# Kernel tuning notes

Hardware: AMD Instinct MI355X
Metric: run time of the kernel (lower is better)

Reference implementation:

```python
import jax, jax.numpy as jnp
import numpy as np

MEM_DIM = 1024
N_CHILD = 16384

def _linear_params(key, out_dim, in_dim):
    kw, kb = jax.random.split(key)
    bound = 1.0 / np.sqrt(in_dim)
    W = jax.random.uniform(kw, (out_dim, in_dim), jnp.float32, -bound, bound)
    b = jax.random.uniform(kb, (out_dim,), jnp.float32, -bound, bound)
    return W, b

def setup_inputs() -> dict:
    key = jax.random.key(0)
    ks = jax.random.split(key, 7)
    child_c = jax.random.normal(ks[0], (N_CHILD, MEM_DIM), jnp.float32)
    child_h = jax.random.normal(ks[1], (N_CHILD, MEM_DIM), jnp.float32)
    child_h_sum = jax.random.normal(ks[2], (MEM_DIM,), jnp.float32)
    W_ih, b_ih = _linear_params(ks[3], MEM_DIM, MEM_DIM)
    W_fh, b_fh = _linear_params(ks[4], MEM_DIM, MEM_DIM)
    W_uh, b_uh = _linear_params(ks[5], MEM_DIM, MEM_DIM)
    W_oh, b_oh = _linear_params(ks[6], MEM_DIM, MEM_DIM)
    return {
        "child_c": child_c, "child_h": child_h, "child_h_sum": child_h_sum,
        "W_ih": W_ih, "b_ih": b_ih, "W_fh": W_fh, "b_fh": b_fh,
        "W_uh": W_uh, "b_uh": b_uh, "W_oh": W_oh, "b_oh": b_oh,
    }

def reference(child_c, child_h, child_h_sum,
              W_ih, b_ih, W_fh, b_fh, W_uh, b_uh, W_oh, b_oh):
    # Gate projections on the summed child hidden state: [mem_dim]
    i = jax.nn.sigmoid(child_h_sum @ W_ih.T + b_ih)
    o = jax.nn.sigmoid(child_h_sum @ W_oh.T + b_oh)
    u = jnp.tanh(child_h_sum @ W_uh.T + b_uh)
    # Per-child forget gates, batched (replaces the Python loop): [N, mem_dim]
    f = jax.nn.sigmoid(child_h @ W_fh.T + b_fh)
    fc = f * child_c                     # [N, mem_dim]
    c = i * u + jnp.sum(fc, axis=0)      # [mem_dim]
    h = o * jnp.tanh(c)                  # [mem_dim]
    return (c, h)
```

## Files before the change

### kernel.cpp

```cpp
#include <hip/hip_runtime.h>
#include <hip/hip_bf16.h>
#include <math.h>

#define MEM_DIM 1024
#define N_CHILD 16384

#define BM 128
#define BN 64
#define BK 64
#define KITERS (MEM_DIM / BK)

typedef __bf16 bf16_t;
typedef __bf16 bf16x4 __attribute__((ext_vector_type(4)));
typedef __bf16 bf16x8 __attribute__((ext_vector_type(8)));
typedef float f32x4 __attribute__((ext_vector_type(4)));

__device__ __forceinline__ void async_load16(const bf16_t* g, bf16_t* l) {
    __builtin_amdgcn_global_load_lds(
        (const __attribute__((address_space(1))) unsigned int*)g,
        (__attribute__((address_space(3))) unsigned int*)l,
        16, 0, 0);
}

__global__ __launch_bounds__(256) void prep_kernel(
        const float* __restrict__ child_h, const float* __restrict__ W_fh,
        bf16_t* __restrict__ dst, int n8,
        const float* __restrict__ hsum,
        const float* __restrict__ W_ih, const float* __restrict__ b_ih,
        const float* __restrict__ W_uh, const float* __restrict__ b_uh,
        const float* __restrict__ W_oh, const float* __restrict__ b_oh,
        float* __restrict__ acc_c, float* __restrict__ o_ws) {
    const int tid = threadIdx.x;
    if (blockIdx.x < MEM_DIM) {
        const int j = blockIdx.x;
        const float* wi = W_ih + (size_t)j * MEM_DIM;
        const float* wu = W_uh + (size_t)j * MEM_DIM;
        const float* wo = W_oh + (size_t)j * MEM_DIM;
        float4 h4  = *(const float4*)(hsum + tid * 4);
        float4 wi4 = *(const float4*)(wi + tid * 4);
        float4 wu4 = *(const float4*)(wu + tid * 4);
        float4 wo4 = *(const float4*)(wo + tid * 4);
        float si = wi4.x * h4.x + wi4.y * h4.y + wi4.z * h4.z + wi4.w * h4.w;
        float su = wu4.x * h4.x + wu4.y * h4.y + wu4.z * h4.z + wu4.w * h4.w;
        float so = wo4.x * h4.x + wo4.y * h4.y + wo4.z * h4.z + wo4.w * h4.w;
        for (int off = 32; off > 0; off >>= 1) {
            si += __shfl_down(si, off, 64);
            su += __shfl_down(su, off, 64);
            so += __shfl_down(so, off, 64);
        }
        __shared__ float red[3][4];
        const int wave = tid >> 6, lane = tid & 63;
        if (lane == 0) { red[0][wave] = si; red[1][wave] = su; red[2][wave] = so; }
        __syncthreads();
        if (tid == 0) {
            float ti = red[0][0] + red[0][1] + red[0][2] + red[0][3] + b_ih[j];
            float tu = red[1][0] + red[1][1] + red[1][2] + red[1][3] + b_uh[j];
            float to = red[2][0] + red[2][1] + red[2][2] + red[2][3] + b_oh[j];
            float iv = 1.f / (1.f + expf(-ti));
            float uv = tanhf(tu);
            float ov = 1.f / (1.f + expf(-to));
            acc_c[j] = iv * uv;
            o_ws[j]  = ov;
        }
    } else {
        const int nA8 = (N_CHILD * MEM_DIM) / 8;
        int t = (blockIdx.x - MEM_DIM) * 256 + tid;
        if (t < n8) {
            const float* s = (t < nA8) ? (child_h + (size_t)t * 8)
                                       : (W_fh + (size_t)(t - nA8) * 8);
            float4 a = *(const float4*)s;
            float4 b = *(const float4*)(s + 4);
            bf16x8 o = { (bf16_t)a.x, (bf16_t)a.y, (bf16_t)a.z, (bf16_t)a.w,
                         (bf16_t)b.x, (bf16_t)b.y, (bf16_t)b.z, (bf16_t)b.w };
            *(bf16x8*)(dst + (size_t)t * 8) = o;
        }
    }
}

__global__ __launch_bounds__(256) void fused_gemm_bf16(
        const bf16_t* __restrict__ hbf, const bf16_t* __restrict__ wbf,
        const float* __restrict__ child_c, const float* __restrict__ b_fh,
        float* __restrict__ acc_c) {
    __shared__ __align__(1024) bf16_t sA[BM * BK];
    __shared__ __align__(1024) bf16_t sB[BN * BK];
    __shared__ float sred[BN];

    const int tid  = threadIdx.x;
    const int lane = tid & 63;
    const int wave = tid >> 6;
    const int wr = wave >> 1;
    const int wc = wave & 1;
    const int q  = lane >> 4;
    const int cl = lane & 15;

    const int b   = blockIdx.x;
    const int xcd = b & 7;
    const int l   = b >> 3;
    const int jt  = l & 15;
    const int ntl = l >> 4;
    const int j0  = jt * BN;
    const int n0  = (xcd * 16 + ntl) * BM;

    const int rl = lane >> 3;
    const int p  = lane & 7;
    const int cf = (p ^ rl) * 8;
    const bf16_t* gA[4];
    bf16_t* lA[4];
#pragma unroll
    for (int i = 0; i < 4; i++) {
        const int r = wave * 32 + i * 8 + rl;
        gA[i] = hbf + (size_t)(n0 + r) * MEM_DIM + cf;
        lA[i] = &sA[(wave * 32 + i * 8) * BK];
    }
    const bf16_t* gB[2];
    bf16_t* lB[2];
#pragma unroll
    for (int i = 0; i < 2; i++) {
        const int r = wave * 16 + i * 8 + rl;
        gB[i] = wbf + (size_t)(j0 + r) * MEM_DIM + cf;
        lB[i] = &sB[(wave * 16 + i * 8) * BK];
    }

    f32x4 acc[4][2];
#pragma unroll
    for (int a = 0; a < 4; a++)
#pragma unroll
        for (int c = 0; c < 2; c++) acc[a][c] = (f32x4)0.0f;

#pragma unroll 1
    for (int k = 0; k < KITERS - 1; ++k) {
#pragma unroll
        for (int i = 0; i < 4; i++) { async_load16(gA[i], lA[i]); gA[i] += BK; }
#pragma unroll
        for (int i = 0; i < 2; i++) { async_load16(gB[i], lB[i]); gB[i] += BK; }
        __syncthreads();

#pragma unroll
        for (int h = 0; h < 2; h++) {
            bf16x8 af[4], bfr[2];
#pragma unroll
            for (int mt = 0; mt < 4; mt++) {
                const int ra = wr * 64 + mt * 16 + cl;
                af[mt] = *(const bf16x8*)(&sA[ra * BK + (((4 * h + q) ^ (cl & 7)) * 8)]);
            }
#pragma unroll
            for (int nt = 0; nt < 2; nt++) {
                const int rb = wc * 32 + nt * 16 + cl;
                bfr[nt] = *(const bf16x8*)(&sB[rb * BK + (((4 * h + q) ^ (cl & 7)) * 8)]);
            }
#pragma unroll
            for (int mt = 0; mt < 4; mt++)
#pragma unroll
                for (int nt = 0; nt < 2; nt++)
                    acc[mt][nt] = __builtin_amdgcn_mfma_f32_16x16x32_bf16(
                        af[mt], bfr[nt], acc[mt][nt], 0, 0, 0);
        }
        __syncthreads();
    }

#pragma unroll
    for (int i = 0; i < 4; i++) async_load16(gA[i], lA[i]);
#pragma unroll
    for (int i = 0; i < 2; i++) async_load16(gB[i], lB[i]);

    float ccr[2][4][4];
    float biasr[2];
    {
        const float* ccp = child_c + (size_t)(n0 + wr * 64 + q * 4) * MEM_DIM
                                   + j0 + wc * 32 + cl;
#pragma unroll
        for (int nt = 0; nt < 2; nt++) {
            biasr[nt] = b_fh[j0 + wc * 32 + nt * 16 + cl];
#pragma unroll
            for (int mt = 0; mt < 4; mt++)
#pragma unroll
                for (int r = 0; r < 4; r++)
                    ccr[nt][mt][r] = ccp[(size_t)(mt * 16 + r) * MEM_DIM + nt * 16];
        }
    }
    __syncthreads();

#pragma unroll
    for (int h = 0; h < 2; h++) {
        bf16x8 af[4], bfr[2];
#pragma unroll
        for (int mt = 0; mt < 4; mt++) {
            const int ra = wr * 64 + mt * 16 + cl;
            af[mt] = *(const bf16x8*)(&sA[ra * BK + (((4 * h + q) ^ (cl & 7)) * 8)]);
        }
#pragma unroll
        for (int nt = 0; nt < 2; nt++) {
            const int rb = wc * 32 + nt * 16 + cl;
            bfr[nt] = *(const bf16x8*)(&sB[rb * BK + (((4 * h + q) ^ (cl & 7)) * 8)]);
        }
#pragma unroll
        for (int mt = 0; mt < 4; mt++)
#pragma unroll
            for (int nt = 0; nt < 2; nt++)
                acc[mt][nt] = __builtin_amdgcn_mfma_f32_16x16x32_bf16(
                    af[mt], bfr[nt], acc[mt][nt], 0, 0, 0);
    }

    if (tid < BN) sred[tid] = 0.0f;
    __syncthreads();

    float colsum[2] = {0.f, 0.f};
#pragma unroll
    for (int nt = 0; nt < 2; nt++) {
#pragma unroll
        for (int mt = 0; mt < 4; mt++) {
#pragma unroll
            for (int r = 0; r < 4; r++) {
                float s = acc[mt][nt][r] + biasr[nt];
                float fg = 1.0f / (1.0f + __expf(-s));
                colsum[nt] += fg * ccr[nt][mt][r];
            }
        }
        colsum[nt] += __shfl_xor(colsum[nt], 16, 64);
        colsum[nt] += __shfl_xor(colsum[nt], 32, 64);
    }
    if (q == 0) {
#pragma unroll
        for (int nt = 0; nt < 2; nt++)
            atomicAdd(&sred[wc * 32 + nt * 16 + cl], colsum[nt]);
    }
    __syncthreads();
    if (tid < BN) atomicAdd(&acc_c[j0 + tid], sred[tid]);
}

__global__ void finalize_kernel(const float* __restrict__ acc_c,
                                const float* __restrict__ o_ws,
                                float* __restrict__ out) {
    int t = blockIdx.x * 256 + threadIdx.x;
    if (t < MEM_DIM) {
        float cv = acc_c[t];
        float hv = o_ws[t] * tanhf(cv);
        out[t] = cv;
        out[MEM_DIM + t] = hv;
    }
}

__global__ void gates_kernel(const float* __restrict__ hsum,
                             const float* __restrict__ W_ih, const float* __restrict__ b_ih,
                             const float* __restrict__ W_uh, const float* __restrict__ b_uh,
                             const float* __restrict__ W_oh, const float* __restrict__ b_oh,
                             float* __restrict__ acc_c, float* __restrict__ o_ws) {
    const int j = blockIdx.x;
    const int tid = threadIdx.x;
    const float* wi = W_ih + (size_t)j * MEM_DIM;
    const float* wu = W_uh + (size_t)j * MEM_DIM;
    const float* wo = W_oh + (size_t)j * MEM_DIM;
    float si = 0.f, su = 0.f, so = 0.f;
    for (int k = tid; k < MEM_DIM; k += 256) {
        float hv = hsum[k];
        si += wi[k] * hv;
        su += wu[k] * hv;
        so += wo[k] * hv;
    }
    for (int off = 32; off > 0; off >>= 1) {
        si += __shfl_down(si, off, 64);
        su += __shfl_down(su, off, 64);
        so += __shfl_down(so, off, 64);
    }
    __shared__ float red[3][4];
    const int wave = tid >> 6, lane = tid & 63;
    if (lane == 0) { red[0][wave] = si; red[1][wave] = su; red[2][wave] = so; }
    __syncthreads();
    if (tid == 0) {
        float ti = red[0][0] + red[0][1] + red[0][2] + red[0][3] + b_ih[j];
        float tu = red[1][0] + red[1][1] + red[1][2] + red[1][3] + b_uh[j];
        float to = red[2][0] + red[2][1] + red[2][2] + red[2][3] + b_oh[j];
        acc_c[j] = (1.f / (1.f + expf(-ti))) * tanhf(tu);
        o_ws[j]  = 1.f / (1.f + expf(-to));
    }
}

#define LDS_STRIDE 40
__global__ __launch_bounds__(256) void fused_gemm_f32(
        const float* __restrict__ child_h, const float* __restrict__ child_c,
        const float* __restrict__ W_fh, const float* __restrict__ b_fh,
        float* __restrict__ acc_c) {
    __shared__ __align__(16) bf16_t sA[128 * LDS_STRIDE];
    __shared__ __align__(16) bf16_t sB[128 * LDS_STRIDE];
    __shared__ float sred[128];
    const int tid = threadIdx.x, lane = tid & 63, wave = tid >> 6;
    const int wr = wave >> 1, wc = wave & 1;
    const int j0 = blockIdx.x * 128, n0 = blockIdx.y * 128;
    const int q = lane >> 4, cl = lane & 15;
    f32x4 acc[4][4];
#pragma unroll
    for (int a = 0; a < 4; a++)
#pragma unroll
        for (int c = 0; c < 4; c++) acc[a][c] = (f32x4)0.0f;
    for (int k0 = 0; k0 < MEM_DIM; k0 += 32) {
#pragma unroll
        for (int i = 0; i < 4; i++) {
            int f = tid + i * 256, row = f >> 3, col = (f & 7) * 4;
            float4 va = *(const float4*)(child_h + (size_t)(n0 + row) * MEM_DIM + k0 + col);
            float4 vb = *(const float4*)(W_fh    + (size_t)(j0 + row) * MEM_DIM + k0 + col);
            bf16x4 ba = { (bf16_t)va.x, (bf16_t)va.y, (bf16_t)va.z, (bf16_t)va.w };
            bf16x4 bb = { (bf16_t)vb.x, (bf16_t)vb.y, (bf16_t)vb.z, (bf16_t)vb.w };
            *(bf16x4*)(&sA[row * LDS_STRIDE + col]) = ba;
            *(bf16x4*)(&sB[row * LDS_STRIDE + col]) = bb;
        }
        __syncthreads();
        bf16x8 af[4], bfr[4];
#pragma unroll
        for (int mt = 0; mt < 4; mt++) {
            af[mt]  = *(const bf16x8*)(&sA[(wr * 64 + mt * 16 + cl) * LDS_STRIDE + q * 8]);
            bfr[mt] = *(const bf16x8*)(&sB[(wc * 64 + mt * 16 + cl) * LDS_STRIDE + q * 8]);
        }
#pragma unroll
        for (int mt = 0; mt < 4; mt++)
#pragma unroll
            for (int nt = 0; nt < 4; nt++)
                acc[mt][nt] = __builtin_amdgcn_mfma_f32_16x16x32_bf16(af[mt], bfr[nt], acc[mt][nt], 0, 0, 0);
        __syncthreads();
    }
    if (tid < 128) sred[tid] = 0.0f;
    __syncthreads();
    float colsum[4] = {0.f, 0.f, 0.f, 0.f};
#pragma unroll
    for (int nt = 0; nt < 4; nt++) {
        const int col = j0 + wc * 64 + nt * 16 + cl;
        const float bias = b_fh[col];
#pragma unroll
        for (int mt = 0; mt < 4; mt++)
#pragma unroll
            for (int r = 0; r < 4; r++) {
                const int row = n0 + wr * 64 + mt * 16 + q * 4 + r;
                float s = acc[mt][nt][r] + bias;
                float fg = 1.0f / (1.0f + __expf(-s));
                colsum[nt] += fg * child_c[(size_t)row * MEM_DIM + col];
            }
        colsum[nt] += __shfl_xor(colsum[nt], 16, 64);
        colsum[nt] += __shfl_xor(colsum[nt], 32, 64);
    }
    if (q == 0)
#pragma unroll
        for (int nt = 0; nt < 4; nt++)
            atomicAdd(&sred[wc * 64 + nt * 16 + cl], colsum[nt]);
    __syncthreads();
    if (tid < 128) atomicAdd(&acc_c[j0 + tid], sred[tid]);
}

extern "C" void kernel_launch(void* const* d_in, const int* in_sizes, int n_in,
                              void* d_out, int out_size, void* d_ws, size_t ws_size,
                              hipStream_t stream) {
    const float* child_c = (const float*)d_in[0];
    const float* child_h = (const float*)d_in[1];
    const float* hsum    = (const float*)d_in[2];
    const float* W_ih    = (const float*)d_in[3];
    const float* b_ih    = (const float*)d_in[4];
    const float* W_fh    = (const float*)d_in[5];
    const float* b_fh    = (const float*)d_in[6];
    const float* W_uh    = (const float*)d_in[7];
    const float* b_uh    = (const float*)d_in[8];
    const float* W_oh    = (const float*)d_in[9];
    const float* b_oh    = (const float*)d_in[10];
    float* out   = (float*)d_out;

    float* acc_c = (float*)d_ws;
    float* o_ws  = acc_c + MEM_DIM;
    const size_t HBF_OFF   = 8192;
    const size_t HBF_BYTES = (size_t)N_CHILD * MEM_DIM * 2;
    const size_t WBF_BYTES = (size_t)MEM_DIM * MEM_DIM * 2;
    const size_t NEED = HBF_OFF + HBF_BYTES + WBF_BYTES;

    if (ws_size >= NEED) {
        bf16_t* hbf = (bf16_t*)((char*)d_ws + HBF_OFF);
        bf16_t* wbf = hbf + (size_t)N_CHILD * MEM_DIM;
        const int n8 = (N_CHILD * MEM_DIM + MEM_DIM * MEM_DIM) / 8;
        const int cvtBlocks = (n8 + 255) / 256;
        prep_kernel<<<MEM_DIM + cvtBlocks, 256, 0, stream>>>(
            child_h, W_fh, hbf, n8,
            hsum, W_ih, b_ih, W_uh, b_uh, W_oh, b_oh, acc_c, o_ws);
        fused_gemm_bf16<<<(N_CHILD / BM) * (MEM_DIM / BN), 256, 0, stream>>>(
            hbf, wbf, child_c, b_fh, acc_c);
    } else {
        gates_kernel<<<MEM_DIM, 256, 0, stream>>>(hsum, W_ih, b_ih, W_uh, b_uh,
                                                  W_oh, b_oh, acc_c, o_ws);
        dim3 grid(MEM_DIM / 128, N_CHILD / 128);
        fused_gemm_f32<<<grid, 256, 0, stream>>>(child_h, child_c, W_fh, b_fh, acc_c);
    }
    finalize_kernel<<<(MEM_DIM + 255) / 256, 256, 0, stream>>>(acc_c, o_ws, out);
}
```

Measured before the change: 211.7 us.

## Fuse fp32-to-bf16 conversion into GEMM loads and use per-tile partial sums

Drops the separate prep pass that converted child_h and W_fh to bf16 in workspace. The GEMM now loads fp32 tiles directly, converts them in registers and writes swizzled bf16 into LDS. The gate-projection blocks are merged into the same launch, and global atomics are replaced by per-row-tile partial sums that the finalize kernel reduces. This avoids writing and re-reading a 32MB bf16 copy but doubles GEMM global read bytes and loses the async global-to-LDS loads. It also adds register pressure from the staged fp32 values.

```diff
diff --git a/kernel.cpp b/kernel.cpp
--- a/kernel.cpp
+++ b/kernel.cpp
@@ -9,28 +9,30 @@
 #define BN 64
 #define BK 64
 #define KITERS (MEM_DIM / BK)
+#define NGEMM ((N_CHILD / BM) * (MEM_DIM / BN))
+#define NPART (N_CHILD / BM)
 
 typedef __bf16 bf16_t;
 typedef __bf16 bf16x4 __attribute__((ext_vector_type(4)));
 typedef __bf16 bf16x8 __attribute__((ext_vector_type(8)));
 typedef float f32x4 __attribute__((ext_vector_type(4)));
 
-__device__ __forceinline__ void async_load16(const bf16_t* g, bf16_t* l) {
-    __builtin_amdgcn_global_load_lds(
-        (const __attribute__((address_space(1))) unsigned int*)g,
-        (__attribute__((address_space(3))) unsigned int*)l,
-        16, 0, 0);
-}
-
-__global__ __launch_bounds__(256) void prep_kernel(
+__global__ __launch_bounds__(256) void fused_main(
         const float* __restrict__ child_h, const float* __restrict__ W_fh,
-        bf16_t* __restrict__ dst, int n8,
+        const float* __restrict__ child_c, const float* __restrict__ b_fh,
         const float* __restrict__ hsum,
         const float* __restrict__ W_ih, const float* __restrict__ b_ih,
         const float* __restrict__ W_uh, const float* __restrict__ b_uh,
         const float* __restrict__ W_oh, const float* __restrict__ b_oh,
-        float* __restrict__ acc_c, float* __restrict__ o_ws) {
+        float* __restrict__ acc_part, float* __restrict__ iu_ws,
+        float* __restrict__ o_ws) {
+    __shared__ __align__(1024) bf16_t sA[BM * BK];
+    __shared__ __align__(1024) bf16_t sB[BN * BK];
+    __shared__ float sred[BN];
+    __shared__ float red[3][4];
+
     const int tid = threadIdx.x;
+
     if (blockIdx.x < MEM_DIM) {
         const int j = blockIdx.x;
         const float* wi = W_ih + (size_t)j * MEM_DIM;
@@ -48,7 +50,6 @@
             su += __shfl_down(su, off, 64);
             so += __shfl_down(so, off, 64);
         }
-        __shared__ float red[3][4];
         const int wave = tid >> 6, lane = tid & 63;
         if (lane == 0) { red[0][wave] = si; red[1][wave] = su; red[2][wave] = so; }
         __syncthreads();
@@ -59,33 +60,13 @@
             float iv = 1.f / (1.f + expf(-ti));
             float uv = tanhf(tu);
             float ov = 1.f / (1.f + expf(-to));
-            acc_c[j] = iv * uv;
+            iu_ws[j] = iv * uv;
             o_ws[j]  = ov;
         }
-    } else {
-        const int nA8 = (N_CHILD * MEM_DIM) / 8;
-        int t = (blockIdx.x - MEM_DIM) * 256 + tid;
-        if (t < n8) {
-            const float* s = (t < nA8) ? (child_h + (size_t)t * 8)
-                                       : (W_fh + (size_t)(t - nA8) * 8);
-            float4 a = *(const float4*)s;
-            float4 b = *(const float4*)(s + 4);
-            bf16x8 o = { (bf16_t)a.x, (bf16_t)a.y, (bf16_t)a.z, (bf16_t)a.w,
-                         (bf16_t)b.x, (bf16_t)b.y, (bf16_t)b.z, (bf16_t)b.w };
-            *(bf16x8*)(dst + (size_t)t * 8) = o;
-        }
-    }
-}
-
-__global__ __launch_bounds__(256) void fused_gemm_bf16(
-        const bf16_t* __restrict__ hbf, const bf16_t* __restrict__ wbf,
-        const float* __restrict__ child_c, const float* __restrict__ b_fh,
-        float* __restrict__ acc_c) {
-    __shared__ __align__(1024) bf16_t sA[BM * BK];
-    __shared__ __align__(1024) bf16_t sB[BN * BK];
-    __shared__ float sred[BN];
-
-    const int tid  = threadIdx.x;
+        return;
+    }
+
+    const int b    = blockIdx.x - MEM_DIM;
     const int lane = tid & 63;
     const int wave = tid >> 6;
     const int wr = wave >> 1;
@@ -93,32 +74,29 @@
     const int q  = lane >> 4;
     const int cl = lane & 15;
 
-    const int b   = blockIdx.x;
     const int xcd = b & 7;
     const int l   = b >> 3;
     const int jt  = l & 15;
     const int ntl = l >> 4;
     const int j0  = jt * BN;
     const int n0  = (xcd * 16 + ntl) * BM;
-
-    const int rl = lane >> 3;
-    const int p  = lane & 7;
-    const int cf = (p ^ rl) * 8;
-    const bf16_t* gA[4];
-    bf16_t* lA[4];
+    const int part = xcd * 16 + ntl;
+
+    const int sr = lane >> 4;
+    const int sc = lane & 15;
+    const float* gA = child_h + (size_t)(n0 + wave * 32 + sr) * MEM_DIM + sc * 4;
+    const float* gB = W_fh    + (size_t)(j0 + wave * 16 + sr) * MEM_DIM + sc * 4;
+
+    int wa[8], wb[4];
+#pragma unroll
+    for (int i = 0; i < 8; i++) {
+        const int r = wave * 32 + i * 4 + sr;
+        wa[i] = r * 128 + ((((sc >> 1) ^ (r & 7)) << 4) | ((sc & 1) << 3));
+    }
 #pragma unroll
     for (int i = 0; i < 4; i++) {
-        const int r = wave * 32 + i * 8 + rl;
-        gA[i] = hbf + (size_t)(n0 + r) * MEM_DIM + cf;
-        lA[i] = &sA[(wave * 32 + i * 8) * BK];
-    }
-    const bf16_t* gB[2];
-    bf16_t* lB[2];
-#pragma unroll
-    for (int i = 0; i < 2; i++) {
-        const int r = wave * 16 + i * 8 + rl;
-        gB[i] = wbf + (size_t)(j0 + r) * MEM_DIM + cf;
-        lB[i] = &sB[(wave * 16 + i * 8) * BK];
+        const int r = wave * 16 + i * 4 + sr;
+        wb[i] = r * 128 + ((((sc >> 1) ^ (r & 7)) << 4) | ((sc & 1) << 3));
     }
 
     f32x4 acc[4][2];
@@ -129,10 +107,27 @@
 
 #pragma unroll 1
     for (int k = 0; k < KITERS - 1; ++k) {
-#pragma unroll
-        for (int i = 0; i < 4; i++) { async_load16(gA[i], lA[i]); gA[i] += BK; }
-#pragma unroll
-        for (int i = 0; i < 2; i++) { async_load16(gB[i], lB[i]); gB[i] += BK; }
+        const int ko = k * BK;
+        float4 a4[8];
+        float4 b4[4];
+#pragma unroll
+        for (int i = 0; i < 8; i++)
+            a4[i] = *(const float4*)(gA + (size_t)i * 4 * MEM_DIM + ko);
+#pragma unroll
+        for (int i = 0; i < 4; i++)
+            b4[i] = *(const float4*)(gB + (size_t)i * 4 * MEM_DIM + ko);
+#pragma unroll
+        for (int i = 0; i < 8; i++) {
+            bf16x4 v = { (bf16_t)a4[i].x, (bf16_t)a4[i].y,
+                         (bf16_t)a4[i].z, (bf16_t)a4[i].w };
+            *(bf16x4*)((char*)sA + wa[i]) = v;
+        }
+#pragma unroll
+        for (int i = 0; i < 4; i++) {
+            bf16x4 v = { (bf16_t)b4[i].x, (bf16_t)b4[i].y,
+                         (bf16_t)b4[i].z, (bf16_t)b4[i].w };
+            *(bf16x4*)((char*)sB + wb[i]) = v;
+        }
         __syncthreads();
 
 #pragma unroll
@@ -158,190 +153,107 @@
         __syncthreads();
     }
 
-#pragma unroll
-    for (int i = 0; i < 4; i++) async_load16(gA[i], lA[i]);
-#pragma unroll
-    for (int i = 0; i < 2; i++) async_load16(gB[i], lB[i]);
-
-    float ccr[2][4][4];
-    float biasr[2];
     {
-        const float* ccp = child_c + (size_t)(n0 + wr * 64 + q * 4) * MEM_DIM
-                                   + j0 + wc * 32 + cl;
+        const int ko = (KITERS - 1) * BK;
+        float4 a4[8];
+        float4 b4[4];
+#pragma unroll
+        for (int i = 0; i < 8; i++)
+            a4[i] = *(const float4*)(gA + (size_t)i * 4 * MEM_DIM + ko);
+#pragma unroll
+        for (int i = 0; i < 4; i++)
+            b4[i] = *(const float4*)(gB + (size_t)i * 4 * MEM_DIM + ko);
+
+        float ccr[2][4][4];
+        float biasr[2];
+        {
+            const float* ccp = child_c + (size_t)(n0 + wr * 64 + q * 4) * MEM_DIM
+                                       + j0 + wc * 32 + cl;
+#pragma unroll
+            for (int nt = 0; nt < 2; nt++) {
+                biasr[nt] = b_fh[j0 + wc * 32 + nt * 16 + cl];
+#pragma unroll
+                for (int mt = 0; mt < 4; mt++)
+#pragma unroll
+                    for (int r = 0; r < 4; r++)
+                        ccr[nt][mt][r] = ccp[(size_t)(mt * 16 + r) * MEM_DIM + nt * 16];
+            }
+        }
+
+#pragma unroll
+        for (int i = 0; i < 8; i++) {
+            bf16x4 v = { (bf16_t)a4[i].x, (bf16_t)a4[i].y,
+                         (bf16_t)a4[i].z, (bf16_t)a4[i].w };
+            *(bf16x4*)((char*)sA + wa[i]) = v;
+        }
+#pragma unroll
+        for (int i = 0; i < 4; i++) {
+            bf16x4 v = { (bf16_t)b4[i].x, (bf16_t)b4[i].y,
+                         (bf16_t)b4[i].z, (bf16_t)b4[i].w };
+            *(bf16x4*)((char*)sB + wb[i]) = v;
+        }
+        __syncthreads();
+
+#pragma unroll
+        for (int h = 0; h < 2; h++) {
+            bf16x8 af[4], bfr[2];
+#pragma unroll
+            for (int mt = 0; mt < 4; mt++) {
+                const int ra = wr * 64 + mt * 16 + cl;
+                af[mt] = *(const bf16x8*)(&sA[ra * BK + (((4 * h + q) ^ (cl & 7)) * 8)]);
+            }
+#pragma unroll
+            for (int nt = 0; nt < 2; nt++) {
+                const int rb = wc * 32 + nt * 16 + cl;
+                bfr[nt] = *(const bf16x8*)(&sB[rb * BK + (((4 * h + q) ^ (cl & 7)) * 8)]);
+            }
+#pragma unroll
+            for (int mt = 0; mt < 4; mt++)
+#pragma unroll
+                for (int nt = 0; nt < 2; nt++)
+                    acc[mt][nt] = __builtin_amdgcn_mfma_f32_16x16x32_bf16(
+                        af[mt], bfr[nt], acc[mt][nt], 0, 0, 0);
+        }
+
+        if (tid < BN) sred[tid] = 0.0f;
+        __syncthreads();
+
+        float colsum[2] = {0.f, 0.f};
 #pragma unroll
         for (int nt = 0; nt < 2; nt++) {
-            biasr[nt] = b_fh[j0 + wc * 32 + nt * 16 + cl];
-#pragma unroll
-            for (int mt = 0; mt < 4; mt++)
-#pragma unroll
-                for (int r = 0; r < 4; r++)
-                    ccr[nt][mt][r] = ccp[(size_t)(mt * 16 + r) * MEM_DIM + nt * 16];
-        }
-    }
-    __syncthreads();
-
-#pragma unroll
-    for (int h = 0; h < 2; h++) {
-        bf16x8 af[4], bfr[2];
-#pragma unroll
-        for (int mt = 0; mt < 4; mt++) {
-            const int ra = wr * 64 + mt * 16 + cl;
-            af[mt] = *(const bf16x8*)(&sA[ra * BK + (((4 * h + q) ^ (cl & 7)) * 8)]);
-        }
-#pragma unroll
-        for (int nt = 0; nt < 2; nt++) {
-            const int rb = wc * 32 + nt * 16 + cl;
-            bfr[nt] = *(const bf16x8*)(&sB[rb * BK + (((4 * h + q) ^ (cl & 7)) * 8)]);
-        }
-#pragma unroll
-        for (int mt = 0; mt < 4; mt++)
+#pragma unroll
+            for (int mt = 0; mt < 4; mt++) {
+#pragma unroll
+                for (int r = 0; r < 4; r++) {
+                    float s = acc[mt][nt][r] + biasr[nt];
+                    float fg = 1.0f / (1.0f + __expf(-s));
+                    colsum[nt] += fg * ccr[nt][mt][r];
+                }
+            }
+            colsum[nt] += __shfl_xor(colsum[nt], 16, 64);
+            colsum[nt] += __shfl_xor(colsum[nt], 32, 64);
+        }
+        if (q == 0) {
 #pragma unroll
             for (int nt = 0; nt < 2; nt++)
-                acc[mt][nt] = __builtin_amdgcn_mfma_f32_16x16x32_bf16(
-                    af[mt], bfr[nt], acc[mt][nt], 0, 0, 0);
-    }
-
-    if (tid < BN) sred[tid] = 0.0f;
-    __syncthreads();
-
-    float colsum[2] = {0.f, 0.f};
-#pragma unroll
-    for (int nt = 0; nt < 2; nt++) {
-#pragma unroll
-        for (int mt = 0; mt < 4; mt++) {
-#pragma unroll
-            for (int r = 0; r < 4; r++) {
-                float s = acc[mt][nt][r] + biasr[nt];
-                float fg = 1.0f / (1.0f + __expf(-s));
-                colsum[nt] += fg * ccr[nt][mt][r];
-            }
-        }
-        colsum[nt] += __shfl_xor(colsum[nt], 16, 64);
-        colsum[nt] += __shfl_xor(colsum[nt], 32, 64);
-    }
-    if (q == 0) {
-#pragma unroll
-        for (int nt = 0; nt < 2; nt++)
-            atomicAdd(&sred[wc * 32 + nt * 16 + cl], colsum[nt]);
-    }
-    __syncthreads();
-    if (tid < BN) atomicAdd(&acc_c[j0 + tid], sred[tid]);
+                atomicAdd(&sred[wc * 32 + nt * 16 + cl], colsum[nt]);
+        }
+        __syncthreads();
+        if (tid < BN)
+            acc_part[(size_t)part * MEM_DIM + j0 + tid] = sred[tid];
+    }
 }
 
-__global__ void finalize_kernel(const float* __restrict__ acc_c,
-                                const float* __restrict__ o_ws,
-                                float* __restrict__ out) {
-    int t = blockIdx.x * 256 + threadIdx.x;
-    if (t < MEM_DIM) {
-        float cv = acc_c[t];
-        float hv = o_ws[t] * tanhf(cv);
-        out[t] = cv;
-        out[MEM_DIM + t] = hv;
-    }
-}
-
-__global__ void gates_kernel(const float* __restrict__ hsum,
-                             const float* __restrict__ W_ih, const float* __restrict__ b_ih,
-                             const float* __restrict__ W_uh, const float* __restrict__ b_uh,
-                             const float* __restrict__ W_oh, const float* __restrict__ b_oh,
-                             float* __restrict__ acc_c, float* __restrict__ o_ws) {
-    const int j = blockIdx.x;
-    const int tid = threadIdx.x;
-    const float* wi = W_ih + (size_t)j * MEM_DIM;
-    const float* wu = W_uh + (size_t)j * MEM_DIM;
-    const float* wo = W_oh + (size_t)j * MEM_DIM;
-    float si = 0.f, su = 0.f, so = 0.f;
-    for (int k = tid; k < MEM_DIM; k += 256) {
-        float hv = hsum[k];
-        si += wi[k] * hv;
-        su += wu[k] * hv;
-        so += wo[k] * hv;
-    }
-    for (int off = 32; off > 0; off >>= 1) {
-        si += __shfl_down(si, off, 64);
-        su += __shfl_down(su, off, 64);
-        so += __shfl_down(so, off, 64);
-    }
-    __shared__ float red[3][4];
-    const int wave = tid >> 6, lane = tid & 63;
-    if (lane == 0) { red[0][wave] = si; red[1][wave] = su; red[2][wave] = so; }
-    __syncthreads();
-    if (tid == 0) {
-        float ti = red[0][0] + red[0][1] + red[0][2] + red[0][3] + b_ih[j];
-        float tu = red[1][0] + red[1][1] + red[1][2] + red[1][3] + b_uh[j];
-        float to = red[2][0] + red[2][1] + red[2][2] + red[2][3] + b_oh[j];
-        acc_c[j] = (1.f / (1.f + expf(-ti))) * tanhf(tu);
-        o_ws[j]  = 1.f / (1.f + expf(-to));
-    }
-}
-
-#define LDS_STRIDE 40
-__global__ __launch_bounds__(256) void fused_gemm_f32(
-        const float* __restrict__ child_h, const float* __restrict__ child_c,
-        const float* __restrict__ W_fh, const float* __restrict__ b_fh,
-        float* __restrict__ acc_c) {
-    __shared__ __align__(16) bf16_t sA[128 * LDS_STRIDE];
-    __shared__ __align__(16) bf16_t sB[128 * LDS_STRIDE];
-    __shared__ float sred[128];
-    const int tid = threadIdx.x, lane = tid & 63, wave = tid >> 6;
-    const int wr = wave >> 1, wc = wave & 1;
-    const int j0 = blockIdx.x * 128, n0 = blockIdx.y * 128;
-    const int q = lane >> 4, cl = lane & 15;
-    f32x4 acc[4][4];
-#pragma unroll
-    for (int a = 0; a < 4; a++)
-#pragma unroll
-        for (int c = 0; c < 4; c++) acc[a][c] = (f32x4)0.0f;
-    for (int k0 = 0; k0 < MEM_DIM; k0 += 32) {
-#pragma unroll
-        for (int i = 0; i < 4; i++) {
-            int f = tid + i * 256, row = f >> 3, col = (f & 7) * 4;
-            float4 va = *(const float4*)(child_h + (size_t)(n0 + row) * MEM_DIM + k0 + col);
-            float4 vb = *(const float4*)(W_fh    + (size_t)(j0 + row) * MEM_DIM + k0 + col);
-            bf16x4 ba = { (bf16_t)va.x, (bf16_t)va.y, (bf16_t)va.z, (bf16_t)va.w };
-            bf16x4 bb = { (bf16_t)vb.x, (bf16_t)vb.y, (bf16_t)vb.z, (bf16_t)vb.w };
-            *(bf16x4*)(&sA[row * LDS_STRIDE + col]) = ba;
-            *(bf16x4*)(&sB[row * LDS_STRIDE + col]) = bb;
-        }
-        __syncthreads();
-        bf16x8 af[4], bfr[4];
-#pragma unroll
-        for (int mt = 0; mt < 4; mt++) {
-            af[mt]  = *(const bf16x8*)(&sA[(wr * 64 + mt * 16 + cl) * LDS_STRIDE + q * 8]);
-            bfr[mt] = *(const bf16x8*)(&sB[(wc * 64 + mt * 16 + cl) * LDS_STRIDE + q * 8]);
-        }
-#pragma unroll
-        for (int mt = 0; mt < 4; mt++)
-#pragma unroll
-            for (int nt = 0; nt < 4; nt++)
-                acc[mt][nt] = __builtin_amdgcn_mfma_f32_16x16x32_bf16(af[mt], bfr[nt], acc[mt][nt], 0, 0, 0);
-        __syncthreads();
-    }
-    if (tid < 128) sred[tid] = 0.0f;
-    __syncthreads();
-    float colsum[4] = {0.f, 0.f, 0.f, 0.f};
-#pragma unroll
-    for (int nt = 0; nt < 4; nt++) {
-        const int col = j0 + wc * 64 + nt * 16 + cl;
-        const float bias = b_fh[col];
-#pragma unroll
-        for (int mt = 0; mt < 4; mt++)
-#pragma unroll
-            for (int r = 0; r < 4; r++) {
-                const int row = n0 + wr * 64 + mt * 16 + q * 4 + r;
-                float s = acc[mt][nt][r] + bias;
-                float fg = 1.0f / (1.0f + __expf(-s));
-                colsum[nt] += fg * child_c[(size_t)row * MEM_DIM + col];
-            }
-        colsum[nt] += __shfl_xor(colsum[nt], 16, 64);
-        colsum[nt] += __shfl_xor(colsum[nt], 32, 64);
-    }
-    if (q == 0)
-#pragma unroll
-        for (int nt = 0; nt < 4; nt++)
-            atomicAdd(&sred[wc * 64 + nt * 16 + cl], colsum[nt]);
-    __syncthreads();
-    if (tid < 128) atomicAdd(&acc_c[j0 + tid], sred[tid]);
+__global__ __launch_bounds__(256) void finalize_kernel(
+        const float* __restrict__ acc_part, const float* __restrict__ iu_ws,
+        const float* __restrict__ o_ws, float* __restrict__ out) {
+    const int j = blockIdx.x * 256 + threadIdx.x;
+    float s = iu_ws[j];
+#pragma unroll 8
+    for (int p = 0; p < NPART; ++p)
+        s += acc_part[(size_t)p * MEM_DIM + j];
+    out[j] = s;
+    out[MEM_DIM + j] = o_ws[j] * tanhf(s);
 }
 
 extern "C" void kernel_launch(void* const* d_in, const int* in_sizes, int n_in,
@@ -358,30 +270,15 @@
     const float* b_uh    = (const float*)d_in[8];
     const float* W_oh    = (const float*)d_in[9];
     const float* b_oh    = (const float*)d_in[10];
-    float* out   = (float*)d_out;
-
-    float* acc_c = (float*)d_ws;
-    float* o_ws  = acc_c + MEM_DIM;
-    const size_t HBF_OFF   = 8192;
-    const size_t HBF_BYTES = (size_t)N_CHILD * MEM_DIM * 2;
-    const size_t WBF_BYTES = (size_t)MEM_DIM * MEM_DIM * 2;
-    const size_t NEED = HBF_OFF + HBF_BYTES + WBF_BYTES;
-
-    if (ws_size >= NEED) {
-        bf16_t* hbf = (bf16_t*)((char*)d_ws + HBF_OFF);
-        bf16_t* wbf = hbf + (size_t)N_CHILD * MEM_DIM;
-        const int n8 = (N_CHILD * MEM_DIM + MEM_DIM * MEM_DIM) / 8;
-        const int cvtBlocks = (n8 + 255) / 256;
-        prep_kernel<<<MEM_DIM + cvtBlocks, 256, 0, stream>>>(
-            child_h, W_fh, hbf, n8,
-            hsum, W_ih, b_ih, W_uh, b_uh, W_oh, b_oh, acc_c, o_ws);
-        fused_gemm_bf16<<<(N_CHILD / BM) * (MEM_DIM / BN), 256, 0, stream>>>(
-            hbf, wbf, child_c, b_fh, acc_c);
-    } else {
-        gates_kernel<<<MEM_DIM, 256, 0, stream>>>(hsum, W_ih, b_ih, W_uh, b_uh,
-                                                  W_oh, b_oh, acc_c, o_ws);
-        dim3 grid(MEM_DIM / 128, N_CHILD / 128);
-        fused_gemm_f32<<<grid, 256, 0, stream>>>(child_h, child_c, W_fh, b_fh, acc_c);
-    }
-    finalize_kernel<<<(MEM_DIM + 255) / 256, 256, 0, stream>>>(acc_c, o_ws, out);
+    float* out = (float*)d_out;
+
+    float* acc_part = (float*)d_ws;
+    float* iu_ws    = acc_part + (size_t)NPART * MEM_DIM;
+    float* o_ws     = iu_ws + MEM_DIM;
+
+    fused_main<<<MEM_DIM + NGEMM, 256, 0, stream>>>(
+        child_h, W_fh, child_c, b_fh,
+        hsum, W_ih, b_ih, W_uh, b_uh, W_oh, b_oh,
+        acc_part, iu_ws, o_ws);
+    finalize_kernel<<<MEM_DIM / 256, 256, 0, stream>>>(acc_part, iu_ws, o_ws, out);
 }
```

After: 243.6 us. 15.1% more time.

## Double-buffer GEMM LDS tiles and replace global atomics with per-tile partials

Applied to the files above, without the earlier changes.

The bf16 GEMM now keeps two LDS buffers and issues the async global-to-LDS loads for the next K tile while MFMAs run on the current one, using a single waitcnt+barrier per iteration instead of two syncthreads. The per-block column sums are written to a partials array indexed by row tile rather than atomically added to acc_c, and a new finalize kernel sums the 128 partials, adds the i*u term and applies tanh. This aims to hide global load latency and remove atomic contention, at the cost of doubled LDS per block (which may lower occupancy) and an extra reduction pass over a 512KB partials buffer.

```diff
diff --git a/kernel.cpp b/kernel.cpp
--- a/kernel.cpp
+++ b/kernel.cpp
@@ -9,6 +9,10 @@
 #define BN 64
 #define BK 64
 #define KITERS (MEM_DIM / BK)
+#define ASZ (BM * BK)
+#define BSZ (BN * BK)
+#define NGEMM ((N_CHILD / BM) * (MEM_DIM / BN))
+#define NPART (N_CHILD / BM)
 
 typedef __bf16 bf16_t;
 typedef __bf16 bf16x4 __attribute__((ext_vector_type(4)));
@@ -80,9 +84,9 @@
 __global__ __launch_bounds__(256) void fused_gemm_bf16(
         const bf16_t* __restrict__ hbf, const bf16_t* __restrict__ wbf,
         const float* __restrict__ child_c, const float* __restrict__ b_fh,
-        float* __restrict__ acc_c) {
-    __shared__ __align__(1024) bf16_t sA[BM * BK];
-    __shared__ __align__(1024) bf16_t sB[BN * BK];
+        float* __restrict__ acc_part) {
+    __shared__ __align__(1024) bf16_t sA[2 * ASZ];
+    __shared__ __align__(1024) bf16_t sB[2 * BSZ];
     __shared__ float sred[BN];
 
     const int tid  = threadIdx.x;
@@ -100,6 +104,7 @@
     const int ntl = l >> 4;
     const int j0  = jt * BN;
     const int n0  = (xcd * 16 + ntl) * BM;
+    const int part = xcd * 16 + ntl;
 
     const int rl = lane >> 3;
     const int p  = lane & 7;
@@ -127,26 +132,37 @@
 #pragma unroll
         for (int c = 0; c < 2; c++) acc[a][c] = (f32x4)0.0f;
 
+#pragma unroll
+    for (int i = 0; i < 4; i++) { async_load16(gA[i], lA[i]); gA[i] += BK; }
+#pragma unroll
+    for (int i = 0; i < 2; i++) { async_load16(gB[i], lB[i]); gB[i] += BK; }
+    asm volatile("s_waitcnt vmcnt(0)" ::: "memory");
+    __builtin_amdgcn_s_barrier();
+    asm volatile("" ::: "memory");
+
+    int cur = 0;
 #pragma unroll 1
-    for (int k = 0; k < KITERS - 1; ++k) {
-#pragma unroll
-        for (int i = 0; i < 4; i++) { async_load16(gA[i], lA[i]); gA[i] += BK; }
-#pragma unroll
-        for (int i = 0; i < 2; i++) { async_load16(gB[i], lB[i]); gB[i] += BK; }
-        __syncthreads();
-
+    for (int t = 0; t < KITERS - 1; ++t) {
+        const int nxt = cur ^ 1;
+#pragma unroll
+        for (int i = 0; i < 4; i++) { async_load16(gA[i], lA[i] + nxt * ASZ); gA[i] += BK; }
+#pragma unroll
+        for (int i = 0; i < 2; i++) { async_load16(gB[i], lB[i] + nxt * BSZ); gB[i] += BK; }
+
+        const bf16_t* cA = sA + cur * ASZ;
+        const bf16_t* cB = sB + cur * BSZ;
 #pragma unroll
         for (int h = 0; h < 2; h++) {
             bf16x8 af[4], bfr[2];
 #pragma unroll
             for (int mt = 0; mt < 4; mt++) {
                 const int ra = wr * 64 + mt * 16 + cl;
-                af[mt] = *(const bf16x8*)(&sA[ra * BK + (((4 * h + q) ^ (cl & 7)) * 8)]);
+                af[mt] = *(const bf16x8*)(&cA[ra * BK + (((4 * h + q) ^ (cl & 7)) * 8)]);
             }
 #pragma unroll
             for (int nt = 0; nt < 2; nt++) {
                 const int rb = wc * 32 + nt * 16 + cl;
-                bfr[nt] = *(const bf16x8*)(&sB[rb * BK + (((4 * h + q) ^ (cl & 7)) * 8)]);
+                bfr[nt] = *(const bf16x8*)(&cB[rb * BK + (((4 * h + q) ^ (cl & 7)) * 8)]);
             }
 #pragma unroll
             for (int mt = 0; mt < 4; mt++)
@@ -155,13 +171,11 @@
                     acc[mt][nt] = __builtin_amdgcn_mfma_f32_16x16x32_bf16(
                         af[mt], bfr[nt], acc[mt][nt], 0, 0, 0);
         }
-        __syncthreads();
-    }
-
-#pragma unroll
-    for (int i = 0; i < 4; i++) async_load16(gA[i], lA[i]);
-#pragma unroll
-    for (int i = 0; i < 2; i++) async_load16(gB[i], lB[i]);
+        asm volatile("s_waitcnt vmcnt(0)" ::: "memory");
+        __builtin_amdgcn_s_barrier();
+        asm volatile("" ::: "memory");
+        cur = nxt;
+    }
 
     float ccr[2][4][4];
     float biasr[2];
@@ -178,27 +192,29 @@
                     ccr[nt][mt][r] = ccp[(size_t)(mt * 16 + r) * MEM_DIM + nt * 16];
         }
     }
-    __syncthreads();
-
-#pragma unroll
-    for (int h = 0; h < 2; h++) {
-        bf16x8 af[4], bfr[2];
-#pragma unroll
-        for (int mt = 0; mt < 4; mt++) {
-            const int ra = wr * 64 + mt * 16 + cl;
-            af[mt] = *(const bf16x8*)(&sA[ra * BK + (((4 * h + q) ^ (cl & 7)) * 8)]);
-        }
-#pragma unroll
-        for (int nt = 0; nt < 2; nt++) {
-            const int rb = wc * 32 + nt * 16 + cl;
-            bfr[nt] = *(const bf16x8*)(&sB[rb * BK + (((4 * h + q) ^ (cl & 7)) * 8)]);
-        }
-#pragma unroll
-        for (int mt = 0; mt < 4; mt++)
-#pragma unroll
-            for (int nt = 0; nt < 2; nt++)
-                acc[mt][nt] = __builtin_amdgcn_mfma_f32_16x16x32_bf16(
-                    af[mt], bfr[nt], acc[mt][nt], 0, 0, 0);
+    {
+        const bf16_t* cA = sA + cur * ASZ;
+        const bf16_t* cB = sB + cur * BSZ;
+#pragma unroll
+        for (int h = 0; h < 2; h++) {
+            bf16x8 af[4], bfr[2];
+#pragma unroll
+            for (int mt = 0; mt < 4; mt++) {
+                const int ra = wr * 64 + mt * 16 + cl;
+                af[mt] = *(const bf16x8*)(&cA[ra * BK + (((4 * h + q) ^ (cl & 7)) * 8)]);
+            }
+#pragma unroll
+            for (int nt = 0; nt < 2; nt++) {
+                const int rb = wc * 32 + nt * 16 + cl;
+                bfr[nt] = *(const bf16x8*)(&cB[rb * BK + (((4 * h + q) ^ (cl & 7)) * 8)]);
+            }
+#pragma unroll
+            for (int mt = 0; mt < 4; mt++)
+#pragma unroll
+                for (int nt = 0; nt < 2; nt++)
+                    acc[mt][nt] = __builtin_amdgcn_mfma_f32_16x16x32_bf16(
+                        af[mt], bfr[nt], acc[mt][nt], 0, 0, 0);
+        }
     }
 
     if (tid < BN) sred[tid] = 0.0f;
@@ -225,19 +241,20 @@
             atomicAdd(&sred[wc * 32 + nt * 16 + cl], colsum[nt]);
     }
     __syncthreads();
-    if (tid < BN) atomicAdd(&acc_c[j0 + tid], sred[tid]);
-}
-
-__global__ void finalize_kernel(const float* __restrict__ acc_c,
-                                const float* __restrict__ o_ws,
-                                float* __restrict__ out) {
-    int t = blockIdx.x * 256 + threadIdx.x;
-    if (t < MEM_DIM) {
-        float cv = acc_c[t];
-        float hv = o_ws[t] * tanhf(cv);
-        out[t] = cv;
-        out[MEM_DIM + t] = hv;
-    }
+    if (tid < BN)
+        acc_part[(size_t)part * MEM_DIM + j0 + tid] = sred[tid];
+}
+
+__global__ __launch_bounds__(256) void finalize2(
+        const float* __restrict__ acc_part, const float* __restrict__ iu_ws,
+        const float* __restrict__ o_ws, float* __restrict__ out) {
+    const int j = blockIdx.x * 256 + threadIdx.x;
+    float s = iu_ws[j];
+#pragma unroll 8
+    for (int p = 0; p < NPART; ++p)
+        s += acc_part[(size_t)p * MEM_DIM + j];
+    out[j] = s;
+    out[MEM_DIM + j] = o_ws[j] * tanhf(s);
 }
 
 __global__ void gates_kernel(const float* __restrict__ hsum,
@@ -344,6 +361,18 @@
     if (tid < 128) atomicAdd(&acc_c[j0 + tid], sred[tid]);
 }
 
+__global__ void finalize_old(const float* __restrict__ acc_c,
+                             const float* __restrict__ o_ws,
+                             float* __restrict__ out) {
+    int t = blockIdx.x * 256 + threadIdx.x;
+    if (t < MEM_DIM) {
+        float cv = acc_c[t];
+        float hv = o_ws[t] * tanhf(cv);
+        out[t] = cv;
+        out[MEM_DIM + t] = hv;
+    }
+}
+
 extern "C" void kernel_launch(void* const* d_in, const int* in_sizes, int n_in,
                               void* d_out, int out_size, void* d_ws, size_t ws_size,
                               hipStream_t stream) {
@@ -365,23 +394,25 @@
     const size_t HBF_OFF   = 8192;
     const size_t HBF_BYTES = (size_t)N_CHILD * MEM_DIM * 2;
     const size_t WBF_BYTES = (size_t)MEM_DIM * MEM_DIM * 2;
-    const size_t NEED = HBF_OFF + HBF_BYTES + WBF_BYTES;
+    const size_t PART_BYTES = (size_t)NPART * MEM_DIM * 4;
+    const size_t NEED = HBF_OFF + HBF_BYTES + WBF_BYTES + PART_BYTES;
 
     if (ws_size >= NEED) {
         bf16_t* hbf = (bf16_t*)((char*)d_ws + HBF_OFF);
         bf16_t* wbf = hbf + (size_t)N_CHILD * MEM_DIM;
+        float* acc_part = (float*)(wbf + (size_t)MEM_DIM * MEM_DIM);
         const int n8 = (N_CHILD * MEM_DIM + MEM_DIM * MEM_DIM) / 8;
         const int cvtBlocks = (n8 + 255) / 256;
         prep_kernel<<<MEM_DIM + cvtBlocks, 256, 0, stream>>>(
             child_h, W_fh, hbf, n8,
             hsum, W_ih, b_ih, W_uh, b_uh, W_oh, b_oh, acc_c, o_ws);
-        fused_gemm_bf16<<<(N_CHILD / BM) * (MEM_DIM / BN), 256, 0, stream>>>(
-            hbf, wbf, child_c, b_fh, acc_c);
+        fused_gemm_bf16<<<NGEMM, 256, 0, stream>>>(hbf, wbf, child_c, b_fh, acc_part);
+        finalize2<<<MEM_DIM / 256, 256, 0, stream>>>(acc_part, acc_c, o_ws, out);
     } else {
         gates_kernel<<<MEM_DIM, 256, 0, stream>>>(hsum, W_ih, b_ih, W_uh, b_uh,
                                                   W_oh, b_oh, acc_c, o_ws);
         dim3 grid(MEM_DIM / 128, N_CHILD / 128);
         fused_gemm_f32<<<grid, 256, 0, stream>>>(child_h, child_c, W_fh, b_fh, acc_c);
-    }
-    finalize_kernel<<<(MEM_DIM + 255) / 256, 256, 0, stream>>>(acc_c, o_ws, out);
-}
+        finalize_old<<<(MEM_DIM + 255) / 256, 256, 0, stream>>>(acc_c, o_ws, out);
+    }
+}
```

After: 224.4 us. +6.0%, slower.
